# Optimization experiments

Measured on AMD Instinct MI355X. Metric: run time of the kernel, lower is better.

Reference implementation:

```python
import jax, jax.numpy as jnp
import numpy as np

B, N, D = 8192, 1024, 3


def setup_inputs() -> dict:
    key = jax.random.key(0)
    k1, k2, k3, k4 = jax.random.split(key, 4)
    return {
        "x": jax.random.normal(k1, (B, N, D), dtype=jnp.float32),
        "mu_x": jax.random.normal(k2, (B, D), dtype=jnp.float32),
        "y": jax.random.normal(k3, (B, N, D), dtype=jnp.float32),
        "mu_y": jax.random.normal(k4, (B, D), dtype=jnp.float32),
    }


def reference(x, mu_x, y, mu_y):
    # Center both point clouds: [B, N, 3]
    xc = x - mu_x[:, None, :]
    yc = y - mu_y[:, None, :]
    # Cross-covariance per batch: [B, 3, 3]
    cov = jnp.einsum('bnd,bne->bde', xc, yc)
    # Batched 3x3 SVD; square matrices so full_matrices=False matches torch
    U, S, Vt = jnp.linalg.svd(cov, full_matrices=False)
    R = jnp.matmul(U, Vt)  # [B, 3, 3] (no det sign correction, as in source)
    # Frobenius norm over (points, dims) per batch
    xn = jnp.sqrt(jnp.sum(xc * xc, axis=(1, 2)))
    yn = jnp.sqrt(jnp.sum(yc * yc, axis=(1, 2)))
    scale_factor_S = yn / (xn + 1e-6)  # [B]
    # Translation: t = mu_y - R @ mu_x
    t = mu_y - jnp.einsum('bij,bj->bi', R, mu_x)  # [B, 3]
    return (R, t, scale_factor_S)
```

## Files before the change

kernel.cpp:

```cpp
#include <hip/hip_runtime.h>

#define NB 8192
#define NPTS 1024
#define NTHREADS 256
#define PPT (NPTS / NTHREADS)


__global__ __launch_bounds__(NTHREADS) void align_kernel(
    const float* __restrict__ x, const float* __restrict__ mu_x,
    const float* __restrict__ y, const float* __restrict__ mu_y,
    float* __restrict__ out)
{
    const int b   = blockIdx.x;
    const int tid = threadIdx.x;

    const float4* x4 = (const float4*)(x + (size_t)b * (NPTS * 3)) + 3 * tid;
    const float4* y4 = (const float4*)(y + (size_t)b * (NPTS * 3)) + 3 * tid;

    const float4 xa = x4[0], xb4 = x4[1], xc4 = x4[2];
    const float4 ya = y4[0], yb4 = y4[1], yc4 = y4[2];

    const float mx0 = mu_x[b * 3 + 0], mx1 = mu_x[b * 3 + 1], mx2 = mu_x[b * 3 + 2];
    const float my0 = mu_y[b * 3 + 0], my1 = mu_y[b * 3 + 1], my2 = mu_y[b * 3 + 2];

    const float xp[4][3] = {{xa.x, xa.y, xa.z}, {xa.w, xb4.x, xb4.y},
                            {xb4.z, xb4.w, xc4.x}, {xc4.y, xc4.z, xc4.w}};
    const float yp[4][3] = {{ya.x, ya.y, ya.z}, {ya.w, yb4.x, yb4.y},
                            {yb4.z, yb4.w, yc4.x}, {yc4.y, yc4.z, yc4.w}};

    float v[11];
    #pragma unroll
    for (int i = 0; i < 11; ++i) v[i] = 0.0f;

    #pragma unroll
    for (int k = 0; k < PPT; ++k) {
        const float xd0 = xp[k][0] - mx0, xd1 = xp[k][1] - mx1, xd2 = xp[k][2] - mx2;
        const float yd0 = yp[k][0] - my0, yd1 = yp[k][1] - my1, yd2 = yp[k][2] - my2;
        v[0] += xd0 * yd0; v[1] += xd0 * yd1; v[2] += xd0 * yd2;
        v[3] += xd1 * yd0; v[4] += xd1 * yd1; v[5] += xd1 * yd2;
        v[6] += xd2 * yd0; v[7] += xd2 * yd1; v[8] += xd2 * yd2;
        v[9]  += xd0 * xd0 + xd1 * xd1 + xd2 * xd2;
        v[10] += yd0 * yd0 + yd1 * yd1 + yd2 * yd2;
    }

    #pragma unroll
    for (int off = 32; off >= 1; off >>= 1) {
        #pragma unroll
        for (int i = 0; i < 11; ++i) v[i] += __shfl_xor(v[i], off, 64);
    }

    __shared__ float sred[4][11];
    const int wave = tid >> 6;
    const int lane = tid & 63;
    if (lane == 0) {
        #pragma unroll
        for (int i = 0; i < 11; ++i) sred[wave][i] = v[i];
    }
    __syncthreads();

    if (tid == 0) {
        float a[11];
        #pragma unroll
        for (int i = 0; i < 11; ++i)
            a[i] = sred[0][i] + sred[1][i] + sred[2][i] + sred[3][i];

        float Q[9];
        #pragma unroll
        for (int i = 0; i < 9; ++i) Q[i] = a[i];

        #pragma unroll
        for (int it = 0; it < 9; ++it) {
            float C[9];
            C[0] = Q[4] * Q[8] - Q[5] * Q[7];
            C[1] = Q[5] * Q[6] - Q[3] * Q[8];
            C[2] = Q[3] * Q[7] - Q[4] * Q[6];
            C[3] = Q[2] * Q[7] - Q[1] * Q[8];
            C[4] = Q[0] * Q[8] - Q[2] * Q[6];
            C[5] = Q[1] * Q[6] - Q[0] * Q[7];
            C[6] = Q[1] * Q[5] - Q[2] * Q[4];
            C[7] = Q[2] * Q[3] - Q[0] * Q[5];
            C[8] = Q[0] * Q[4] - Q[1] * Q[3];
            const float det = Q[0] * C[0] + Q[1] * C[1] + Q[2] * C[2];
            const float invdet = 1.0f / det;

            float nq = 0.0f, nc = 0.0f;
            #pragma unroll
            for (int i = 0; i < 9; ++i) { nq += Q[i] * Q[i]; nc += C[i] * C[i]; }
            const float g  = sqrtf(sqrtf(nc * invdet * invdet / nq));
            const float hg = 0.5f * g;
            const float hi = 0.5f * invdet / g;
            #pragma unroll
            for (int i = 0; i < 9; ++i) Q[i] = hg * Q[i] + hi * C[i];
        }

        #pragma unroll
        for (int i = 0; i < 9; ++i) out[(size_t)b * 9 + i] = Q[i];

        float* tout = out + (size_t)NB * 9 + (size_t)b * 3;
        tout[0] = my0 - (Q[0] * mx0 + Q[1] * mx1 + Q[2] * mx2);
        tout[1] = my1 - (Q[3] * mx0 + Q[4] * mx1 + Q[5] * mx2);
        tout[2] = my2 - (Q[6] * mx0 + Q[7] * mx1 + Q[8] * mx2);

        out[(size_t)NB * 12 + b] = sqrtf(a[10]) / (sqrtf(a[9]) + 1e-6f);
    }
}

extern "C" void kernel_launch(void* const* d_in, const int* in_sizes, int n_in,
                              void* d_out, int out_size, void* d_ws, size_t ws_size,
                              hipStream_t stream) {
    const float* x    = (const float*)d_in[0];
    const float* mu_x = (const float*)d_in[1];
    const float* y    = (const float*)d_in[2];
    const float* mu_y = (const float*)d_in[3];
    float* out = (float*)d_out;
    align_kernel<<<dim3(NB), dim3(NTHREADS), 0, stream>>>(x, mu_x, y, mu_y, out);
}
```

Baseline: 224.2 us.

## Split into wave-per-batch covariance kernel and thread-per-batch polar kernel

Result: faster. 219.8 us (-2.0%).

```diff
diff --git a/kernel.cpp b/kernel.cpp
--- a/kernel.cpp
+++ b/kernel.cpp
@@ -2,45 +2,48 @@
 
 #define NB 8192
 #define NPTS 1024
-#define NTHREADS 256
-#define PPT (NPTS / NTHREADS)
 
 
-__global__ __launch_bounds__(NTHREADS) void align_kernel(
-    const float* __restrict__ x, const float* __restrict__ mu_x,
-    const float* __restrict__ y, const float* __restrict__ mu_y,
-    float* __restrict__ out)
+__global__ __launch_bounds__(256) void cov_kernel(
+    const float* __restrict__ x, const float* __restrict__ y,
+    const float* __restrict__ mu_x, const float* __restrict__ mu_y,
+    float* __restrict__ ws)
 {
-    const int b   = blockIdx.x;
-    const int tid = threadIdx.x;
+    const int wave = threadIdx.x >> 6;
+    const int lane = threadIdx.x & 63;
+    const int b    = blockIdx.x * 4 + wave;
 
-    const float4* x4 = (const float4*)(x + (size_t)b * (NPTS * 3)) + 3 * tid;
-    const float4* y4 = (const float4*)(y + (size_t)b * (NPTS * 3)) + 3 * tid;
-
-    const float4 xa = x4[0], xb4 = x4[1], xc4 = x4[2];
-    const float4 ya = y4[0], yb4 = y4[1], yc4 = y4[2];
+    const float4* x4 = (const float4*)(x + (size_t)b * (NPTS * 3));
+    const float4* y4 = (const float4*)(y + (size_t)b * (NPTS * 3));
 
     const float mx0 = mu_x[b * 3 + 0], mx1 = mu_x[b * 3 + 1], mx2 = mu_x[b * 3 + 2];
     const float my0 = mu_y[b * 3 + 0], my1 = mu_y[b * 3 + 1], my2 = mu_y[b * 3 + 2];
-
-    const float xp[4][3] = {{xa.x, xa.y, xa.z}, {xa.w, xb4.x, xb4.y},
-                            {xb4.z, xb4.w, xc4.x}, {xc4.y, xc4.z, xc4.w}};
-    const float yp[4][3] = {{ya.x, ya.y, ya.z}, {ya.w, yb4.x, yb4.y},
-                            {yb4.z, yb4.w, yc4.x}, {yc4.y, yc4.z, yc4.w}};
 
     float v[11];
     #pragma unroll
     for (int i = 0; i < 11; ++i) v[i] = 0.0f;
 
     #pragma unroll
-    for (int k = 0; k < PPT; ++k) {
-        const float xd0 = xp[k][0] - mx0, xd1 = xp[k][1] - mx1, xd2 = xp[k][2] - mx2;
-        const float yd0 = yp[k][0] - my0, yd1 = yp[k][1] - my1, yd2 = yp[k][2] - my2;
-        v[0] += xd0 * yd0; v[1] += xd0 * yd1; v[2] += xd0 * yd2;
-        v[3] += xd1 * yd0; v[4] += xd1 * yd1; v[5] += xd1 * yd2;
-        v[6] += xd2 * yd0; v[7] += xd2 * yd1; v[8] += xd2 * yd2;
-        v[9]  += xd0 * xd0 + xd1 * xd1 + xd2 * xd2;
-        v[10] += yd0 * yd0 + yd1 * yd1 + yd2 * yd2;
+    for (int c = 0; c < 4; ++c) {
+        const int base = 3 * (c * 64 + lane);
+        const float4 xa = x4[base + 0], xb4 = x4[base + 1], xc4 = x4[base + 2];
+        const float4 ya = y4[base + 0], yb4 = y4[base + 1], yc4 = y4[base + 2];
+
+        const float xp[4][3] = {{xa.x, xa.y, xa.z}, {xa.w, xb4.x, xb4.y},
+                                {xb4.z, xb4.w, xc4.x}, {xc4.y, xc4.z, xc4.w}};
+        const float yp[4][3] = {{ya.x, ya.y, ya.z}, {ya.w, yb4.x, yb4.y},
+                                {yb4.z, yb4.w, yc4.x}, {yc4.y, yc4.z, yc4.w}};
+
+        #pragma unroll
+        for (int k = 0; k < 4; ++k) {
+            const float xd0 = xp[k][0] - mx0, xd1 = xp[k][1] - mx1, xd2 = xp[k][2] - mx2;
+            const float yd0 = yp[k][0] - my0, yd1 = yp[k][1] - my1, yd2 = yp[k][2] - my2;
+            v[0] += xd0 * yd0; v[1] += xd0 * yd1; v[2] += xd0 * yd2;
+            v[3] += xd1 * yd0; v[4] += xd1 * yd1; v[5] += xd1 * yd2;
+            v[6] += xd2 * yd0; v[7] += xd2 * yd1; v[8] += xd2 * yd2;
+            v[9]  += xd0 * xd0 + xd1 * xd1 + xd2 * xd2;
+            v[10] += yd0 * yd0 + yd1 * yd1 + yd2 * yd2;
+        }
     }
 
     #pragma unroll
@@ -49,60 +52,64 @@
         for (int i = 0; i < 11; ++i) v[i] += __shfl_xor(v[i], off, 64);
     }
 
-    __shared__ float sred[4][11];
-    const int wave = tid >> 6;
-    const int lane = tid & 63;
     if (lane == 0) {
+        float* w = ws + (size_t)b * 12;
         #pragma unroll
-        for (int i = 0; i < 11; ++i) sred[wave][i] = v[i];
+        for (int i = 0; i < 11; ++i) w[i] = v[i];
     }
-    __syncthreads();
+}
 
-    if (tid == 0) {
-        float a[11];
+__global__ __launch_bounds__(256) void polar_kernel(
+    const float* __restrict__ ws,
+    const float* __restrict__ mu_x, const float* __restrict__ mu_y,
+    float* __restrict__ out)
+{
+    const int b = blockIdx.x * 256 + threadIdx.x;
+
+    const float4* w4 = (const float4*)ws + 3 * (size_t)b;
+    const float4 w0 = w4[0], w1 = w4[1], w2 = w4[2];
+
+    float Q[9] = {w0.x, w0.y, w0.z, w0.w, w1.x, w1.y, w1.z, w1.w, w2.x};
+    const float nxx = w2.y;
+    const float nyy = w2.z;
+
+    #pragma unroll
+    for (int it = 0; it < 11; ++it) {
+        float C[9];
+        C[0] = Q[4] * Q[8] - Q[5] * Q[7];
+        C[1] = Q[5] * Q[6] - Q[3] * Q[8];
+        C[2] = Q[3] * Q[7] - Q[4] * Q[6];
+        C[3] = Q[2] * Q[7] - Q[1] * Q[8];
+        C[4] = Q[0] * Q[8] - Q[2] * Q[6];
+        C[5] = Q[1] * Q[6] - Q[0] * Q[7];
+        C[6] = Q[1] * Q[5] - Q[2] * Q[4];
+        C[7] = Q[2] * Q[3] - Q[0] * Q[5];
+        C[8] = Q[0] * Q[4] - Q[1] * Q[3];
+        const float det = Q[0] * C[0] + Q[1] * C[1] + Q[2] * C[2];
+        const float invdet = 1.0f / det;
+
+        float nq = 0.0f, nc = 0.0f;
         #pragma unroll
-        for (int i = 0; i < 11; ++i)
-            a[i] = sred[0][i] + sred[1][i] + sred[2][i] + sred[3][i];
+        for (int i = 0; i < 9; ++i) { nq += Q[i] * Q[i]; nc += C[i] * C[i]; }
+        const float g  = sqrtf(sqrtf(nc * invdet * invdet / nq));
+        const float hg = 0.5f * g;
+        const float hi = 0.5f * invdet / g;
+        #pragma unroll
+        for (int i = 0; i < 9; ++i) Q[i] = hg * Q[i] + hi * C[i];
+    }
 
-        float Q[9];
-        #pragma unroll
-        for (int i = 0; i < 9; ++i) Q[i] = a[i];
+    const float mx0 = mu_x[b * 3 + 0], mx1 = mu_x[b * 3 + 1], mx2 = mu_x[b * 3 + 2];
+    const float my0 = mu_y[b * 3 + 0], my1 = mu_y[b * 3 + 1], my2 = mu_y[b * 3 + 2];
 
-        #pragma unroll
-        for (int it = 0; it < 9; ++it) {
-            float C[9];
-            C[0] = Q[4] * Q[8] - Q[5] * Q[7];
-            C[1] = Q[5] * Q[6] - Q[3] * Q[8];
-            C[2] = Q[3] * Q[7] - Q[4] * Q[6];
-            C[3] = Q[2] * Q[7] - Q[1] * Q[8];
-            C[4] = Q[0] * Q[8] - Q[2] * Q[6];
-            C[5] = Q[1] * Q[6] - Q[0] * Q[7];
-            C[6] = Q[1] * Q[5] - Q[2] * Q[4];
-            C[7] = Q[2] * Q[3] - Q[0] * Q[5];
-            C[8] = Q[0] * Q[4] - Q[1] * Q[3];
-            const float det = Q[0] * C[0] + Q[1] * C[1] + Q[2] * C[2];
-            const float invdet = 1.0f / det;
+    #pragma unroll
+    for (int i = 0; i < 9; ++i) out[(size_t)b * 9 + i] = Q[i];
 
-            float nq = 0.0f, nc = 0.0f;
-            #pragma unroll
-            for (int i = 0; i < 9; ++i) { nq += Q[i] * Q[i]; nc += C[i] * C[i]; }
-            const float g  = sqrtf(sqrtf(nc * invdet * invdet / nq));
-            const float hg = 0.5f * g;
-            const float hi = 0.5f * invdet / g;
-            #pragma unroll
-            for (int i = 0; i < 9; ++i) Q[i] = hg * Q[i] + hi * C[i];
-        }
+    float* tout = out + (size_t)NB * 9 + (size_t)b * 3;
+    tout[0] = my0 - (Q[0] * mx0 + Q[1] * mx1 + Q[2] * mx2);
+    tout[1] = my1 - (Q[3] * mx0 + Q[4] * mx1 + Q[5] * mx2);
+    tout[2] = my2 - (Q[6] * mx0 + Q[7] * mx1 + Q[8] * mx2);
 
-        #pragma unroll
-        for (int i = 0; i < 9; ++i) out[(size_t)b * 9 + i] = Q[i];
-
-        float* tout = out + (size_t)NB * 9 + (size_t)b * 3;
-        tout[0] = my0 - (Q[0] * mx0 + Q[1] * mx1 + Q[2] * mx2);
-        tout[1] = my1 - (Q[3] * mx0 + Q[4] * mx1 + Q[5] * mx2);
-        tout[2] = my2 - (Q[6] * mx0 + Q[7] * mx1 + Q[8] * mx2);
-
-        out[(size_t)NB * 12 + b] = sqrtf(a[10]) / (sqrtf(a[9]) + 1e-6f);
-    }
+    out[(size_t)NB * 12 + b] = sqrtf(nyy) / (sqrtf(nxx) + 1e-6f);
 }
 
 extern "C" void kernel_launch(void* const* d_in, const int* in_sizes, int n_in,
@@ -113,5 +120,8 @@
     const float* y    = (const float*)d_in[2];
     const float* mu_y = (const float*)d_in[3];
     float* out = (float*)d_out;
-    align_kernel<<<dim3(NB), dim3(NTHREADS), 0, stream>>>(x, mu_x, y, mu_y, out);
+    float* ws  = (float*)d_ws;
+
+    cov_kernel<<<dim3(NB / 4), dim3(256), 0, stream>>>(x, y, mu_x, mu_y, ws);
+    polar_kernel<<<dim3(NB / 256), dim3(256), 0, stream>>>(ws, mu_x, mu_y, out);
 }
```
